# Performance work log

Measured on AMD Instinct MI355X. Metric: run time of the kernel, lower is better.

Reference implementation:

```python
import jax, jax.numpy as jnp
import numpy as np
import math

B, S, E, H = 2, 4096, 1024, 1024

def setup_inputs() -> dict:
    key = jax.random.key(0)
    ks = jax.random.split(key, 7)
    X = jax.random.normal(ks[0], (B, S, E), dtype=jnp.float32)
    attention_mask = jnp.ones((B, S, S), dtype=jnp.int32)
    sc = 1.0 / math.sqrt(E)
    Wq = jax.random.normal(ks[1], (H, E), dtype=jnp.float32) * sc
    Wk = jax.random.normal(ks[2], (H, E), dtype=jnp.float32) * sc
    Wv = jax.random.normal(ks[3], (H, E), dtype=jnp.float32) * sc
    bq = jnp.zeros((H,), dtype=jnp.float32)
    bk = jnp.zeros((H,), dtype=jnp.float32)
    bv = jnp.zeros((H,), dtype=jnp.float32)
    return {"X": X, "attention_mask": attention_mask,
            "Wq": Wq, "bq": bq, "Wk": Wk, "bk": bk, "Wv": Wv, "bv": bv}

def reference(X, attention_mask, Wq, bq, Wk, bk, Wv, bv):
    # Linear layers: y = x @ W^T + b (torch convention W is [out, in])
    Q = jnp.einsum('bse,he->bsh', X, Wq) + bq
    K = jnp.einsum('bse,he->bsh', X, Wk) + bk
    V = jnp.einsum('bse,he->bsh', X, Wv) + bv
    scale = 1.0 / math.sqrt(H)
    scores = jnp.einsum('bqh,bkh->bqk', Q, K) * scale  # [B,S,S]
    scores = jnp.where(attention_mask == 0, -jnp.inf, scores)
    # dropout (eval mode -> identity) would be applied here, BEFORE softmax
    weights = jax.nn.softmax(scores, axis=-1)
    out = jnp.einsum('bqk,bkh->bqh', weights, V)  # [B,S,H]
    return out
```

## Files before the change

kernel.cpp:

```cpp
#include <hip/hip_runtime.h>
#include <stdint.h>


typedef __bf16 bf16;
typedef __attribute__((ext_vector_type(8))) __bf16 bf16x8;
typedef __attribute__((ext_vector_type(4))) float f32x4;
typedef __attribute__((ext_vector_type(4))) int i32x4;

__device__ __forceinline__ void g2l16(const void* g, void* l) {
  __builtin_amdgcn_global_load_lds(
      (const __attribute__((address_space(1))) uint32_t*)g,
      (__attribute__((address_space(3))) uint32_t*)l, 16, 0, 0);
}

__global__ __launch_bounds__(256) void cvt_f32_bf16(
    const float* __restrict__ src, bf16* __restrict__ dst, int n) {
  const int i = (blockIdx.x * 256 + threadIdx.x) * 8;
  if (i >= n) return;
  f32x4 a = *(const f32x4*)(src + i);
  f32x4 b = *(const f32x4*)(src + i + 4);
  bf16x8 o;
#pragma unroll
  for (int e = 0; e < 4; ++e) { o[e] = (bf16)a[e]; o[4 + e] = (bf16)b[e]; }
  *(bf16x8*)(dst + i) = o;
}

__global__ __launch_bounds__(256, 2) void gemm_qkv(
    const bf16* __restrict__ Xb, const bf16* __restrict__ Wb3,
    const float* __restrict__ bq, const float* __restrict__ bk,
    const float* __restrict__ bv, bf16* __restrict__ OutBase)
{
  constexpr int K = 1024, N = 1024;
  __shared__ __align__(16) bf16 ldsA[128 * 64];
  __shared__ __align__(16) bf16 ldsB[128 * 64];

  const int tid  = threadIdx.x;
  const int lane = tid & 63;
  const int wave = tid >> 6;
  const int which = blockIdx.x >> 3;
  const int n0 = (blockIdx.x & 7) * 128;
  const int m0 = blockIdx.y * 128;
  const bf16* Bt = Wb3 + (size_t)which * 1048576;
  bf16* C = OutBase + (size_t)which * (size_t)(8192 * 1024);
  const float* bias = (which == 0) ? bq : ((which == 1) ? bk : bv);

  const int l15  = lane & 15;
  const int quad = lane >> 4;
  const int wm = (wave >> 1) * 64;
  const int wn = (wave & 1) * 64;

  f32x4 acc[4][4];
#pragma unroll
  for (int i = 0; i < 4; ++i)
#pragma unroll
    for (int j = 0; j < 4; ++j) acc[i][j] = f32x4{0.f, 0.f, 0.f, 0.f};

  const int srow = tid >> 3;
  const int scol = (tid & 7) * 8;
  const size_t a_base = (size_t)(m0 + srow) * K + scol;
  const size_t b_base = (size_t)(n0 + srow) * K + scol;
  const int lds_off = tid * 8;

  for (int kt = 0; kt < K; kt += 64) {
    const bf16* ga = Xb + a_base + kt;
    const bf16* gb = Bt + b_base + kt;
#pragma unroll
    for (int it = 0; it < 4; ++it) {
      g2l16(ga + (size_t)(it * 32) * K, &ldsA[lds_off + it * 2048]);
      g2l16(gb + (size_t)(it * 32) * K, &ldsB[lds_off + it * 2048]);
    }
    __syncthreads();
#pragma unroll
    for (int ks = 0; ks < 2; ++ks) {
      const int ko = ks * 32 + quad * 8;
      bf16x8 af[4], bfg[4];
#pragma unroll
      for (int i = 0; i < 4; ++i)
        af[i] = *(const bf16x8*)&ldsA[(wm + i * 16 + l15) * 64 + ko];
#pragma unroll
      for (int j = 0; j < 4; ++j)
        bfg[j] = *(const bf16x8*)&ldsB[(wn + j * 16 + l15) * 64 + ko];
#pragma unroll
      for (int i = 0; i < 4; ++i)
#pragma unroll
        for (int j = 0; j < 4; ++j)
          acc[i][j] = __builtin_amdgcn_mfma_f32_16x16x32_bf16(
              af[i], bfg[j], acc[i][j], 0, 0, 0);
    }
    __syncthreads();
  }

#pragma unroll
  for (int i = 0; i < 4; ++i) {
#pragma unroll
    for (int j = 0; j < 4; ++j) {
      const int r = m0 + wm + i * 16 + quad * 4;
      const int c = n0 + wn + j * 16 + l15;
      const float bvv = bias[c];
      f32x4 v = acc[i][j];
#pragma unroll
      for (int reg = 0; reg < 4; ++reg)
        C[(size_t)(r + reg) * N + c] = (bf16)(v[reg] + bvv);
    }
  }
}

template <typename CT>
__global__ __launch_bounds__(256, 2) void gemm_bt(
    const bf16* __restrict__ A, const bf16* __restrict__ Bt,
    CT* __restrict__ C, int M, int N, int K, long long bt_batch_stride,
    float scale)
{
  __shared__ __align__(16) bf16 ldsA[128 * 64];
  __shared__ __align__(16) bf16 ldsB[128 * 64];

  const int tid  = threadIdx.x;
  const int lane = tid & 63;
  const int wave = tid >> 6;
  const int m0 = blockIdx.y * 128;
  const int n0 = blockIdx.x * 128;
  const int batch = m0 >> 12;
  const bf16* Btb = Bt + (size_t)batch * (size_t)bt_batch_stride;

  const int l15  = lane & 15;
  const int quad = lane >> 4;
  const int wm = (wave >> 1) * 64;
  const int wn = (wave & 1) * 64;

  f32x4 acc[4][4];
#pragma unroll
  for (int i = 0; i < 4; ++i)
#pragma unroll
    for (int j = 0; j < 4; ++j) acc[i][j] = f32x4{0.f, 0.f, 0.f, 0.f};

  const int srow = tid >> 3;
  const int scol = (tid & 7) * 8;
  const size_t a_base = (size_t)(m0 + srow) * K + scol;
  const size_t b_base = (size_t)(n0 + srow) * K + scol;
  const int lds_off = tid * 8;

  for (int kt = 0; kt < K; kt += 64) {
    const bf16* ga = A + a_base + kt;
    const bf16* gb = Btb + b_base + kt;
#pragma unroll
    for (int it = 0; it < 4; ++it) {
      g2l16(ga + (size_t)(it * 32) * K, &ldsA[lds_off + it * 2048]);
      g2l16(gb + (size_t)(it * 32) * K, &ldsB[lds_off + it * 2048]);
    }
    __syncthreads();
#pragma unroll
    for (int ks = 0; ks < 2; ++ks) {
      const int ko = ks * 32 + quad * 8;
      bf16x8 af[4], bfg[4];
#pragma unroll
      for (int i = 0; i < 4; ++i)
        af[i] = *(const bf16x8*)&ldsA[(wm + i * 16 + l15) * 64 + ko];
#pragma unroll
      for (int j = 0; j < 4; ++j)
        bfg[j] = *(const bf16x8*)&ldsB[(wn + j * 16 + l15) * 64 + ko];
#pragma unroll
      for (int i = 0; i < 4; ++i)
#pragma unroll
        for (int j = 0; j < 4; ++j)
          acc[i][j] = __builtin_amdgcn_mfma_f32_16x16x32_bf16(
              af[i], bfg[j], acc[i][j], 0, 0, 0);
    }
    __syncthreads();
  }

#pragma unroll
  for (int i = 0; i < 4; ++i) {
#pragma unroll
    for (int j = 0; j < 4; ++j) {
      const int r = m0 + wm + i * 16 + quad * 4;
      const int c = n0 + wn + j * 16 + l15;
      f32x4 v = acc[i][j];
#pragma unroll
      for (int reg = 0; reg < 4; ++reg)
        C[(size_t)(r + reg) * N + c] = (CT)(v[reg] * scale);
    }
  }
}

__global__ __launch_bounds__(256) void transpose_v(const bf16* __restrict__ V,
                                                   bf16* __restrict__ Vt) {
  __shared__ bf16 t[32][33];
  const int b = blockIdx.z;
  const int h0 = blockIdx.x * 32;
  const int s0 = blockIdx.y * 32;
  const int tx = threadIdx.x & 31;
  const int ty = threadIdx.x >> 5;
#pragma unroll
  for (int p = 0; p < 4; ++p) {
    const int ls = p * 8 + ty;
    t[ls][tx] = V[((size_t)b * 4096 + s0 + ls) * 1024 + h0 + tx];
  }
  __syncthreads();
#pragma unroll
  for (int p = 0; p < 4; ++p) {
    const int lh = p * 8 + ty;
    Vt[((size_t)b * 1024 + h0 + lh) * 4096 + s0 + tx] = t[tx][lh];
  }
}

__global__ __launch_bounds__(256) void softmax_rows(
    bf16* __restrict__ Sc, const int* __restrict__ mask) {
  const int row = blockIdx.x;
  bf16* p = Sc + (size_t)row * 4096;
  const int* mrow = mask + (size_t)row * 4096;
  const int tid = threadIdx.x;
  const int wave = tid >> 6;

  const bf16x8* pv = (const bf16x8*)p;
  bf16x8 v0 = pv[tid * 2];
  bf16x8 v1 = pv[tid * 2 + 1];
  const i32x4* mv = (const i32x4*)mrow;
  i32x4 mk[4];
#pragma unroll
  for (int q = 0; q < 4; ++q) mk[q] = mv[tid * 4 + q];

  float x[16];
#pragma unroll
  for (int i = 0; i < 8; ++i) {
    x[i] = (float)v0[i];
    x[8 + i] = (float)v1[i];
  }
#pragma unroll
  for (int i = 0; i < 16; ++i)
    if (mk[i >> 2][i & 3] == 0) x[i] = -30000.0f;

  float m = -30000.0f;
#pragma unroll
  for (int i = 0; i < 16; ++i) m = fmaxf(m, x[i]);
#pragma unroll
  for (int off = 1; off < 64; off <<= 1) m = fmaxf(m, __shfl_xor(m, off));
  __shared__ float red[4];
  if ((tid & 63) == 0) red[wave] = m;
  __syncthreads();
  m = fmaxf(fmaxf(red[0], red[1]), fmaxf(red[2], red[3]));

  float s = 0.f;
#pragma unroll
  for (int i = 0; i < 16; ++i) {
    x[i] = __expf(x[i] - m);
    s += x[i];
  }
#pragma unroll
  for (int off = 1; off < 64; off <<= 1) s += __shfl_xor(s, off);
  __syncthreads();
  if ((tid & 63) == 0) red[wave] = s;
  __syncthreads();
  s = red[0] + red[1] + red[2] + red[3];
  const float inv = 1.0f / s;

  bf16x8 o0, o1;
#pragma unroll
  for (int i = 0; i < 8; ++i) {
    o0[i] = (bf16)(x[i] * inv);
    o1[i] = (bf16)(x[8 + i] * inv);
  }
  bf16x8* pw = (bf16x8*)p;
  pw[tid * 2] = o0;
  pw[tid * 2 + 1] = o1;
}

extern "C" void kernel_launch(void* const* d_in, const int* in_sizes, int n_in,
                              void* d_out, int out_size, void* d_ws,
                              size_t ws_size, hipStream_t stream) {
  const float* X   = (const float*)d_in[0];
  const int* mask  = (const int*)d_in[1];
  const float* Wq  = (const float*)d_in[2];
  const float* bq  = (const float*)d_in[3];
  const float* Wk  = (const float*)d_in[4];
  const float* bk  = (const float*)d_in[5];
  const float* Wv  = (const float*)d_in[6];
  const float* bv  = (const float*)d_in[7];
  float* out = (float*)d_out;

  const size_t QKV_ELEMS = (size_t)8192 * 1024;
  bf16* Q    = (bf16*)d_ws;
  bf16* Kb   = Q + QKV_ELEMS;
  bf16* V    = Kb + QKV_ELEMS;
  bf16* Vt   = V + QKV_ELEMS;
  bf16* Sc   = Vt + QKV_ELEMS;
  bf16* X_bf = Sc;
  bf16* W_bf = Sc + QKV_ELEMS;

  const dim3 blk(256);
  cvt_f32_bf16<<<dim3(8388608 / 2048), blk, 0, stream>>>(X, X_bf, 8388608);
  cvt_f32_bf16<<<dim3(512), blk, 0, stream>>>(Wq, W_bf, 1048576);
  cvt_f32_bf16<<<dim3(512), blk, 0, stream>>>(Wk, W_bf + 1048576, 1048576);
  cvt_f32_bf16<<<dim3(512), blk, 0, stream>>>(Wv, W_bf + 2097152, 1048576);
  gemm_qkv<<<dim3(24, 64), blk, 0, stream>>>(X_bf, W_bf, bq, bk, bv, Q);
  transpose_v<<<dim3(32, 128, 2), blk, 0, stream>>>(V, Vt);
  gemm_bt<bf16><<<dim3(32, 64), blk, 0, stream>>>(
      Q, Kb, Sc, 8192, 4096, 1024, 4096LL * 1024LL, 0.03125f);
  softmax_rows<<<dim3(8192), blk, 0, stream>>>(Sc, mask);
  gemm_bt<float><<<dim3(8, 64), blk, 0, stream>>>(
      Sc, Vt, out, 8192, 1024, 4096, 1024LL * 4096LL, 1.0f);
}
```

Measured before the change: 478.2 us.

## Fuse V transpose into QKV GEMM epilogue, merge weight casts, swap grid order

The V output of the QKV projection is now written directly in transposed layout from the GEMM epilogue using 4-wide bf16 stores. This removes the separate transpose kernel and its extra read and write of V. The three weight conversion launches are merged into one kernel. The grid dimensions are swapped so consecutive blocks walk along M and share the same B tile, which may improve L2 reuse. The transposed stores are strided by 4096 elements per column, which could make the epilogue writes less coalesced.

```diff
diff --git a/kernel.cpp b/kernel.cpp
--- a/kernel.cpp
+++ b/kernel.cpp
@@ -3,6 +3,7 @@
 
 
 typedef __bf16 bf16;
+typedef __attribute__((ext_vector_type(4))) __bf16 bf16x4;
 typedef __attribute__((ext_vector_type(8))) __bf16 bf16x8;
 typedef __attribute__((ext_vector_type(4))) float f32x4;
 typedef __attribute__((ext_vector_type(4))) int i32x4;
@@ -25,10 +26,26 @@
   *(bf16x8*)(dst + i) = o;
 }
 
+__global__ __launch_bounds__(256) void cvt_w3(
+    const float* __restrict__ Wq, const float* __restrict__ Wk,
+    const float* __restrict__ Wv, bf16* __restrict__ dst) {
+  const int i = (blockIdx.x * 256 + threadIdx.x) * 8;
+  const int seg = i >> 20;
+  const int off = i & 1048575;
+  const float* src = (seg == 0) ? Wq : (seg == 1) ? Wk : Wv;
+  f32x4 a = *(const f32x4*)(src + off);
+  f32x4 b = *(const f32x4*)(src + off + 4);
+  bf16x8 o;
+#pragma unroll
+  for (int e = 0; e < 4; ++e) { o[e] = (bf16)a[e]; o[4 + e] = (bf16)b[e]; }
+  *(bf16x8*)(dst + i) = o;
+}
+
 __global__ __launch_bounds__(256, 2) void gemm_qkv(
     const bf16* __restrict__ Xb, const bf16* __restrict__ Wb3,
     const float* __restrict__ bq, const float* __restrict__ bk,
-    const float* __restrict__ bv, bf16* __restrict__ OutBase)
+    const float* __restrict__ bv, bf16* __restrict__ QK,
+    bf16* __restrict__ Vt)
 {
   constexpr int K = 1024, N = 1024;
   __shared__ __align__(16) bf16 ldsA[128 * 64];
@@ -37,11 +54,10 @@
   const int tid  = threadIdx.x;
   const int lane = tid & 63;
   const int wave = tid >> 6;
-  const int which = blockIdx.x >> 3;
-  const int n0 = (blockIdx.x & 7) * 128;
-  const int m0 = blockIdx.y * 128;
+  const int which = blockIdx.y >> 3;
+  const int n0 = (blockIdx.y & 7) * 128;
+  const int m0 = blockIdx.x * 128;
   const bf16* Bt = Wb3 + (size_t)which * 1048576;
-  bf16* C = OutBase + (size_t)which * (size_t)(8192 * 1024);
   const float* bias = (which == 0) ? bq : ((which == 1) ? bk : bv);
 
   const int l15  = lane & 15;
@@ -90,17 +106,36 @@
     __syncthreads();
   }
 
-#pragma unroll
-  for (int i = 0; i < 4; ++i) {
-#pragma unroll
-    for (int j = 0; j < 4; ++j) {
-      const int r = m0 + wm + i * 16 + quad * 4;
-      const int c = n0 + wn + j * 16 + l15;
-      const float bvv = bias[c];
-      f32x4 v = acc[i][j];
-#pragma unroll
-      for (int reg = 0; reg < 4; ++reg)
-        C[(size_t)(r + reg) * N + c] = (bf16)(v[reg] + bvv);
+  if (which < 2) {
+    bf16* C = QK + (size_t)which * (size_t)(8192 * 1024);
+#pragma unroll
+    for (int i = 0; i < 4; ++i) {
+#pragma unroll
+      for (int j = 0; j < 4; ++j) {
+        const int r = m0 + wm + i * 16 + quad * 4;
+        const int c = n0 + wn + j * 16 + l15;
+        const float bvv = bias[c];
+        f32x4 v = acc[i][j];
+#pragma unroll
+        for (int reg = 0; reg < 4; ++reg)
+          C[(size_t)(r + reg) * N + c] = (bf16)(v[reg] + bvv);
+      }
+    }
+  } else {
+#pragma unroll
+    for (int i = 0; i < 4; ++i) {
+#pragma unroll
+      for (int j = 0; j < 4; ++j) {
+        const int r = m0 + wm + i * 16 + quad * 4;
+        const int c = n0 + wn + j * 16 + l15;
+        const int b = r >> 12, s = r & 4095;
+        const float bvv = bias[c];
+        f32x4 v = acc[i][j];
+        bf16x4 o;
+#pragma unroll
+        for (int reg = 0; reg < 4; ++reg) o[reg] = (bf16)(v[reg] + bvv);
+        *(bf16x4*)&Vt[((size_t)(b * 1024 + c)) * 4096 + s] = o;
+      }
     }
   }
 }
@@ -117,8 +152,8 @@
   const int tid  = threadIdx.x;
   const int lane = tid & 63;
   const int wave = tid >> 6;
-  const int m0 = blockIdx.y * 128;
-  const int n0 = blockIdx.x * 128;
+  const int m0 = blockIdx.x * 128;
+  const int n0 = blockIdx.y * 128;
   const int batch = m0 >> 12;
   const bf16* Btb = Bt + (size_t)batch * (size_t)bt_batch_stride;
 
@@ -179,27 +214,6 @@
       for (int reg = 0; reg < 4; ++reg)
         C[(size_t)(r + reg) * N + c] = (CT)(v[reg] * scale);
     }
-  }
-}
-
-__global__ __launch_bounds__(256) void transpose_v(const bf16* __restrict__ V,
-                                                   bf16* __restrict__ Vt) {
-  __shared__ bf16 t[32][33];
-  const int b = blockIdx.z;
-  const int h0 = blockIdx.x * 32;
-  const int s0 = blockIdx.y * 32;
-  const int tx = threadIdx.x & 31;
-  const int ty = threadIdx.x >> 5;
-#pragma unroll
-  for (int p = 0; p < 4; ++p) {
-    const int ls = p * 8 + ty;
-    t[ls][tx] = V[((size_t)b * 4096 + s0 + ls) * 1024 + h0 + tx];
-  }
-  __syncthreads();
-#pragma unroll
-  for (int p = 0; p < 4; ++p) {
-    const int lh = p * 8 + ty;
-    Vt[((size_t)b * 1024 + h0 + lh) * 4096 + s0 + tx] = t[tx][lh];
   }
 }
 
@@ -280,22 +294,18 @@
   const size_t QKV_ELEMS = (size_t)8192 * 1024;
   bf16* Q    = (bf16*)d_ws;
   bf16* Kb   = Q + QKV_ELEMS;
-  bf16* V    = Kb + QKV_ELEMS;
-  bf16* Vt   = V + QKV_ELEMS;
+  bf16* X_bf = Kb + QKV_ELEMS;
+  bf16* Vt   = X_bf + QKV_ELEMS;
   bf16* Sc   = Vt + QKV_ELEMS;
-  bf16* X_bf = Sc;
-  bf16* W_bf = Sc + QKV_ELEMS;
+  bf16* W_bf = Sc;
 
   const dim3 blk(256);
-  cvt_f32_bf16<<<dim3(8388608 / 2048), blk, 0, stream>>>(X, X_bf, 8388608);
-  cvt_f32_bf16<<<dim3(512), blk, 0, stream>>>(Wq, W_bf, 1048576);
-  cvt_f32_bf16<<<dim3(512), blk, 0, stream>>>(Wk, W_bf + 1048576, 1048576);
-  cvt_f32_bf16<<<dim3(512), blk, 0, stream>>>(Wv, W_bf + 2097152, 1048576);
-  gemm_qkv<<<dim3(24, 64), blk, 0, stream>>>(X_bf, W_bf, bq, bk, bv, Q);
-  transpose_v<<<dim3(32, 128, 2), blk, 0, stream>>>(V, Vt);
-  gemm_bt<bf16><<<dim3(32, 64), blk, 0, stream>>>(
+  cvt_f32_bf16<<<dim3(4096), blk, 0, stream>>>(X, X_bf, 8388608);
+  cvt_w3<<<dim3(1536), blk, 0, stream>>>(Wq, Wk, Wv, W_bf);
+  gemm_qkv<<<dim3(64, 24), blk, 0, stream>>>(X_bf, W_bf, bq, bk, bv, Q, Vt);
+  gemm_bt<bf16><<<dim3(64, 32), blk, 0, stream>>>(
       Q, Kb, Sc, 8192, 4096, 1024, 4096LL * 1024LL, 0.03125f);
   softmax_rows<<<dim3(8192), blk, 0, stream>>>(Sc, mask);
-  gemm_bt<float><<<dim3(8, 64), blk, 0, stream>>>(
+  gemm_bt<float><<<dim3(64, 8), blk, 0, stream>>>(
       Sc, Vt, out, 8192, 1024, 4096, 1024LL * 4096LL, 1.0f);
 }
```

After: 468.6 us. -2.0%, faster.
